# Kernel tuning notes

Measured on AMD Instinct MI355X. Metric: run time of the kernel, lower is better.

The kernel has to match this reference:

```python
import jax, jax.numpy as jnp
import numpy as np

F = 16        # num_frames
K = 8         # num_tokens (top-k)
SIZE = 64     # basis size
PD = 256      # prompt_dim
ED = 768      # embed_dim
EPS = 1e-12

def _l2norm(v, axis=-1):
    n = jnp.sqrt(jnp.sum(v * v, axis=axis, keepdims=True))
    return v / jnp.maximum(n, EPS)

def setup_inputs() -> dict:
    key = jax.random.key(0)
    k1, k2, k3, k4 = jax.random.split(key, 4)
    B, N = 32, 197
    x = jax.random.normal(k1, (B, F * N, ED), dtype=jnp.float32)
    # prompt_values ~ U(-1, 1), shape [size, 1, prompt_dim]
    prompt_values = jax.random.uniform(k2, (SIZE, 1, PD), dtype=jnp.float32, minval=-1.0, maxval=1.0)
    # prompt_inproj: Linear(embed_dim, prompt_dim, bias=False)
    W_in = jax.random.normal(k3, (PD, ED), dtype=jnp.float32) * (1.0 / np.sqrt(ED))
    # prompt_outproj: Linear(prompt_dim, embed_dim, bias=False), kaiming fan_out
    W_out = jax.random.normal(k4, (ED, PD), dtype=jnp.float32) * np.sqrt(2.0 / ED)
    return {"x": x, "W_in": W_in, "W_out": W_out, "prompt_values": prompt_values}

def reference(x, W_in, W_out, prompt_values):
    B = x.shape[0]
    x = jax.lax.stop_gradient(x)                       # x.detach()
    xf = x.reshape(B, F, -1, ED).mean(axis=2)          # [B, F, ED]
    query = jnp.einsum('bfe,pe->bfp', xf, W_in)        # prompt_inproj
    BZ = B * F
    q = _l2norm(query.reshape(BZ, PD), axis=1)         # [BZ, PD]
    keys = _l2norm(prompt_values.mean(axis=1), axis=1) # [SIZE, PD]
    sim = q @ keys.T                                   # [BZ, SIZE]
    # eval routing: top-k by similarity (argsort descending [:, :k])
    _, idx = jax.lax.top_k(sim, K)                     # [BZ, K] int32
    prompts = prompt_values[idx.reshape(-1)].reshape(BZ, K, PD)
    prompts = _l2norm(prompts, axis=-1)
    sel_sim = jnp.take_along_axis(sim, idx, axis=1)    # [BZ, K]
    sel_key = keys[idx]                                # [BZ, K, PD]
    recon = jnp.einsum('bk,bkd->bd', sel_sim, sel_key) # [BZ, PD]
    diff = jnp.sum((recon - jax.lax.stop_gradient(q)) ** 2) / BZ
    ksim = jnp.sum(jnp.abs(keys @ keys.T - jnp.eye(SIZE, dtype=keys.dtype))) / BZ
    ps = diff + ksim
    # rearrange '(b f) p d -> b (f p) d' then outproj
    out_prompts = prompts.reshape(B, F * K, PD)
    out_prompts = jnp.einsum('bnd,ed->bne', out_prompts, W_out)  # [B, F*K, ED]
    ps_loss = jnp.zeros((1,), dtype=x.dtype) + ps * F
    return out_prompts, ps_loss
```

## Files before the change

### kernel.cpp

```cpp
#include <hip/hip_runtime.h>

#define Ff 16
#define Kk 8
#define SIZEk 64
#define PDd 256
#define EDd 768
#define Nn 197
#define BZz 512
#define NPROD 64
#define RB  256
#define ED4 192
#define PD4 64
#define OUT_LOSS ((size_t)32 * 128 * EDd)
#define LOSS_SCALE (1.0f / 32.0f)
#define MAGIC 0x5A17EC0Du

__global__ __launch_bounds__(256, 2) void k_all(const float4* __restrict__ x,
                                                const float* __restrict__ Win,
                                                const float* __restrict__ Wout,
                                                const float* __restrict__ pv,
                                                float* __restrict__ keys,
                                                float* __restrict__ KW,
                                                unsigned* __restrict__ slots,
                                                float* __restrict__ out) {
    int blk = blockIdx.x, t = threadIdx.x;

    if (blk < NPROD) {
        __shared__ float ks[PDd];
        __shared__ float redp[4];
        __shared__ float s_norm;
        int s = blk;
        float v  = pv[(size_t)s * PDd + t];
        float sq = v * v;
        for (int o = 32; o > 0; o >>= 1) sq += __shfl_down(sq, o);
        if ((t & 63) == 0) redp[t >> 6] = sq;
        __syncthreads();
        if (t == 0) s_norm = fmaxf(sqrtf(redp[0] + redp[1] + redp[2] + redp[3]), 1e-12f);
        __syncthreads();
        float kv = v / s_norm;
        ks[t] = kv;
        keys[(size_t)s * PDd + t] = kv;
        __syncthreads();

        for (int r = 0; r < 3; r++) {
            int e = t + 256 * r;
            const float4* w  = (const float4*)(Wout + (size_t)e * PDd);
            const float4* k4 = (const float4*)ks;
            float d = 0.f;
            for (int i = 0; i < PD4; i++) {
                float4 wv = w[i]; float4 kvv = k4[i];
                d += wv.x * kvv.x + wv.y * kvv.y + wv.z * kvv.z + wv.w * kvv.w;
            }
            KW[(size_t)s * EDd + e] = d;
        }
        if (s == 0 && t == 0) out[OUT_LOSS] = 0.0f;
        __syncthreads();
        if (t == 0)
            __hip_atomic_store(&slots[s], MAGIC, __ATOMIC_RELEASE, __HIP_MEMORY_SCOPE_AGENT);

        if (t < SIZEk) {
            while (__hip_atomic_load(&slots[t], __ATOMIC_ACQUIRE, __HIP_MEMORY_SCOPE_AGENT)
                   != MAGIC)
                __builtin_amdgcn_s_sleep(8);
        }
        __syncthreads();
        if (t < SIZEk) {
            const float4* a = (const float4*)(keys + (size_t)s * PDd);
            const float4* b = (const float4*)(keys + (size_t)t * PDd);
            float d = 0.f;
            for (int c = 0; c < PD4; c++) {
                float4 av = a[c], bv = b[c];
                d += av.x * bv.x + av.y * bv.y + av.z * bv.z + av.w * bv.w;
            }
            float vv = fabsf(d - (s == t ? 1.0f : 0.0f));
            for (int o = 32; o > 0; o >>= 1) vv += __shfl_down(vv, o);
            if (t == 0) atomicAdd(out + OUT_LOSS, vv * LOSS_SCALE);
        }
        return;
    }

    __shared__ float xs[2][EDd];
    __shared__ float qs[2][PDd];
    __shared__ int   s_idx[2][Kk];
    __shared__ float s_sim[2][Kk];
    __shared__ float red[2][4];
    int bz0 = (blk - NPROD) * 2;

    if (t < ED4) {
        const float4* b0 = x + (size_t)bz0 * Nn * ED4;
        const float4* b1 = b0 + (size_t)Nn * ED4;
        float4 s0 = make_float4(0.f, 0.f, 0.f, 0.f);
        float4 s1 = make_float4(0.f, 0.f, 0.f, 0.f);
        int n = 0;
        for (; n + 4 <= Nn; n += 4) {
            float4 a0 = b0[(n + 0) * ED4 + t];
            float4 a1 = b0[(n + 1) * ED4 + t];
            float4 a2 = b0[(n + 2) * ED4 + t];
            float4 a3 = b0[(n + 3) * ED4 + t];
            float4 c0 = b1[(n + 0) * ED4 + t];
            float4 c1 = b1[(n + 1) * ED4 + t];
            float4 c2 = b1[(n + 2) * ED4 + t];
            float4 c3 = b1[(n + 3) * ED4 + t];
            s0.x += (a0.x + a1.x) + (a2.x + a3.x);
            s0.y += (a0.y + a1.y) + (a2.y + a3.y);
            s0.z += (a0.z + a1.z) + (a2.z + a3.z);
            s0.w += (a0.w + a1.w) + (a2.w + a3.w);
            s1.x += (c0.x + c1.x) + (c2.x + c3.x);
            s1.y += (c0.y + c1.y) + (c2.y + c3.y);
            s1.z += (c0.z + c1.z) + (c2.z + c3.z);
            s1.w += (c0.w + c1.w) + (c2.w + c3.w);
        }
        for (; n < Nn; n++) {
            float4 a = b0[n * ED4 + t];
            float4 c = b1[n * ED4 + t];
            s0.x += a.x; s0.y += a.y; s0.z += a.z; s0.w += a.w;
            s1.x += c.x; s1.y += c.y; s1.z += c.z; s1.w += c.w;
        }
        const float inv = 1.0f / (float)Nn;
        s0.x *= inv; s0.y *= inv; s0.z *= inv; s0.w *= inv;
        s1.x *= inv; s1.y *= inv; s1.z *= inv; s1.w *= inv;
        ((float4*)xs[0])[t] = s0;
        ((float4*)xs[1])[t] = s1;
    }
    __syncthreads();

    {
        const float4* w  = (const float4*)Win + (size_t)t * ED4;
        const float4* x0 = (const float4*)xs[0];
        const float4* x1 = (const float4*)xs[1];
        float d0 = 0.f, d1 = 0.f;
        for (int i = 0; i < ED4; i++) {
            float4 wv = w[i];
            float4 u0 = x0[i], u1 = x1[i];
            d0 += wv.x * u0.x + wv.y * u0.y + wv.z * u0.z + wv.w * u0.w;
            d1 += wv.x * u1.x + wv.y * u1.y + wv.z * u1.z + wv.w * u1.w;
        }
        float sq0 = d0 * d0, sq1 = d1 * d1;
        for (int o = 32; o > 0; o >>= 1) {
            sq0 += __shfl_down(sq0, o);
            sq1 += __shfl_down(sq1, o);
        }
        if ((t & 63) == 0) { red[0][t >> 6] = sq0; red[1][t >> 6] = sq1; }
        __syncthreads();
        float n0 = fmaxf(sqrtf(red[0][0] + red[0][1] + red[0][2] + red[0][3]), 1e-12f);
        float n1 = fmaxf(sqrtf(red[1][0] + red[1][1] + red[1][2] + red[1][3]), 1e-12f);
        qs[0][t] = d0 / n0;
        qs[1][t] = d1 / n1;
    }

    if (t < SIZEk) {
        while (__hip_atomic_load(&slots[t], __ATOMIC_ACQUIRE, __HIP_MEMORY_SCOPE_AGENT)
               != MAGIC)
            __builtin_amdgcn_s_sleep(8);
    }
    __syncthreads();

    if (t < 2 * SIZEk) {
        int row  = t >> 6;
        int lane = t & 63;
        const float4* kr = (const float4*)(keys + (size_t)lane * PDd);
        const float4* qr = (const float4*)qs[row];
        float d = 0.f;
        for (int c = 0; c < PD4; c++) {
            float4 a = kr[c], b = qr[c];
            d += a.x * b.x + a.y * b.y + a.z * b.z + a.w * b.w;
        }
        float v = d;
        for (int k = 0; k < Kk; k++) {
            float mv = v; int mi = lane;
            for (int o = 32; o > 0; o >>= 1) {
                float ov = __shfl_xor(mv, o);
                int   oi = __shfl_xor(mi, o);
                if (ov > mv || (ov == mv && oi < mi)) { mv = ov; mi = oi; }
            }
            if (lane == 0) { s_idx[row][k] = mi; s_sim[row][k] = mv; }
            if (lane == mi) v = -3e38f;
        }
    }
    __syncthreads();

    {
        float r0 = 0.f, r1 = 0.f;
        for (int k = 0; k < Kk; k++) {
            r0 += s_sim[0][k] * keys[(size_t)s_idx[0][k] * PDd + t];
            r1 += s_sim[1][k] * keys[(size_t)s_idx[1][k] * PDd + t];
        }
        float e0 = r0 - qs[0][t];
        float e1 = r1 - qs[1][t];
        float sq = e0 * e0 + e1 * e1;
        for (int o = 32; o > 0; o >>= 1) sq += __shfl_down(sq, o);
        if ((t & 63) == 0) red[0][t >> 6] = sq;
        __syncthreads();
        if (t == 0) atomicAdd(out + OUT_LOSS,
                              (red[0][0] + red[0][1] + red[0][2] + red[0][3]) * LOSS_SCALE);
    }

    float4* orow = (float4*)out + (size_t)bz0 * Kk * ED4;
    for (int i = t; i < 2 * Kk * ED4; i += 256) {
        int which = i / ED4;
        int e4    = i - which * ED4;
        int idx   = s_idx[which >> 3][which & 7];
        orow[i] = ((const float4*)(KW + (size_t)idx * EDd))[e4];
    }
}

extern "C" void kernel_launch(void* const* d_in, const int* in_sizes, int n_in,
                              void* d_out, int out_size, void* d_ws, size_t ws_size,
                              hipStream_t stream) {
    const float* x    = (const float*)d_in[0];
    const float* Win  = (const float*)d_in[1];
    const float* Wout = (const float*)d_in[2];
    const float* pv   = (const float*)d_in[3];
    float* out = (float*)d_out;
    float* ws  = (float*)d_ws;

    float*    keys  = ws;
    float*    KW    = ws + 16384;
    unsigned* slots = (unsigned*)(ws + 65536);

    k_all<<<NPROD + RB, 256, 0, stream>>>((const float4*)x, Win, Wout, pv,
                                          keys, KW, slots, out);
}
```

Baseline: 470.1 us.

## Assign one frame per block and use all 256 threads for mean reduction

```diff
diff --git a/kernel.cpp b/kernel.cpp
--- a/kernel.cpp
+++ b/kernel.cpp
@@ -1,19 +1,24 @@
 #include <hip/hip_runtime.h>
 
-#define Ff 16
 #define Kk 8
 #define SIZEk 64
 #define PDd 256
 #define EDd 768
 #define Nn 197
-#define BZz 512
 #define NPROD 64
-#define RB  256
+#define NR 512
 #define ED4 192
 #define PD4 64
+#define TOT4 (Nn * ED4)
+#define JFULL (TOT4 / 256)
+#define JMAIN (JFULL - (JFULL % 6))
 #define OUT_LOSS ((size_t)32 * 128 * EDd)
 #define LOSS_SCALE (1.0f / 32.0f)
 #define MAGIC 0x5A17EC0Du
+
+__device__ __forceinline__ void acc4(float4& s, float4 a) {
+    s.x += a.x; s.y += a.y; s.z += a.z; s.w += a.w;
+}
 
 __global__ __launch_bounds__(256, 2) void k_all(const float4* __restrict__ x,
                                                 const float* __restrict__ Win,
@@ -79,73 +84,67 @@
         return;
     }
 
-    __shared__ float xs[2][EDd];
-    __shared__ float qs[2][PDd];
-    __shared__ int   s_idx[2][Kk];
-    __shared__ float s_sim[2][Kk];
-    __shared__ float red[2][4];
-    int bz0 = (blk - NPROD) * 2;
-
+    __shared__ float4 part[4][ED4];
+    __shared__ float4 xs4[ED4];
+    __shared__ float4 qs4[PD4];
+    __shared__ int    s_idx[Kk];
+    __shared__ float  s_sim[Kk];
+    __shared__ float  red[4];
+    int bz = blk - NPROD;
+
+    {
+        const float4* base = x + (size_t)bz * TOT4;
+        float4 a0 = make_float4(0.f, 0.f, 0.f, 0.f);
+        float4 a1 = a0, a2 = a0;
+        int j = 0;
+        for (; j < JMAIN; j += 6) {
+            const float4* p = base + (size_t)j * 256 + t;
+            float4 v0 = p[0 * 256], v1 = p[1 * 256], v2 = p[2 * 256];
+            float4 v3 = p[3 * 256], v4 = p[4 * 256], v5 = p[5 * 256];
+            acc4(a0, v0); acc4(a1, v1); acc4(a2, v2);
+            acc4(a0, v3); acc4(a1, v4); acc4(a2, v5);
+        }
+        int f = JMAIN * 256 + t;
+        if (f < TOT4) acc4(a0, base[f]); f += 256;
+        if (f < TOT4) acc4(a1, base[f]); f += 256;
+        if (f < TOT4) acc4(a2, base[f]); f += 256;
+        if (f < TOT4) acc4(a0, base[f]);
+
+        int k  = t >> 6;
+        int c0 = t % ED4;
+        int c1 = (t + 64) % ED4;
+        int c2 = (t + 128) % ED4;
+        part[k][c0] = a0;
+        part[k][c1] = a1;
+        part[k][c2] = a2;
+    }
+    __syncthreads();
     if (t < ED4) {
-        const float4* b0 = x + (size_t)bz0 * Nn * ED4;
-        const float4* b1 = b0 + (size_t)Nn * ED4;
-        float4 s0 = make_float4(0.f, 0.f, 0.f, 0.f);
-        float4 s1 = make_float4(0.f, 0.f, 0.f, 0.f);
-        int n = 0;
-        for (; n + 4 <= Nn; n += 4) {
-            float4 a0 = b0[(n + 0) * ED4 + t];
-            float4 a1 = b0[(n + 1) * ED4 + t];
-            float4 a2 = b0[(n + 2) * ED4 + t];
-            float4 a3 = b0[(n + 3) * ED4 + t];
-            float4 c0 = b1[(n + 0) * ED4 + t];
-            float4 c1 = b1[(n + 1) * ED4 + t];
-            float4 c2 = b1[(n + 2) * ED4 + t];
-            float4 c3 = b1[(n + 3) * ED4 + t];
-            s0.x += (a0.x + a1.x) + (a2.x + a3.x);
-            s0.y += (a0.y + a1.y) + (a2.y + a3.y);
-            s0.z += (a0.z + a1.z) + (a2.z + a3.z);
-            s0.w += (a0.w + a1.w) + (a2.w + a3.w);
-            s1.x += (c0.x + c1.x) + (c2.x + c3.x);
-            s1.y += (c0.y + c1.y) + (c2.y + c3.y);
-            s1.z += (c0.z + c1.z) + (c2.z + c3.z);
-            s1.w += (c0.w + c1.w) + (c2.w + c3.w);
-        }
-        for (; n < Nn; n++) {
-            float4 a = b0[n * ED4 + t];
-            float4 c = b1[n * ED4 + t];
-            s0.x += a.x; s0.y += a.y; s0.z += a.z; s0.w += a.w;
-            s1.x += c.x; s1.y += c.y; s1.z += c.z; s1.w += c.w;
-        }
+        float4 s = part[0][t];
+        acc4(s, part[1][t]); acc4(s, part[2][t]); acc4(s, part[3][t]);
         const float inv = 1.0f / (float)Nn;
-        s0.x *= inv; s0.y *= inv; s0.z *= inv; s0.w *= inv;
-        s1.x *= inv; s1.y *= inv; s1.z *= inv; s1.w *= inv;
-        ((float4*)xs[0])[t] = s0;
-        ((float4*)xs[1])[t] = s1;
-    }
-    __syncthreads();
-
+        xs4[t] = make_float4(s.x * inv, s.y * inv, s.z * inv, s.w * inv);
+    }
+    __syncthreads();
+
+    float qv;
     {
-        const float4* w  = (const float4*)Win + (size_t)t * ED4;
-        const float4* x0 = (const float4*)xs[0];
-        const float4* x1 = (const float4*)xs[1];
-        float d0 = 0.f, d1 = 0.f;
-        for (int i = 0; i < ED4; i++) {
-            float4 wv = w[i];
-            float4 u0 = x0[i], u1 = x1[i];
-            d0 += wv.x * u0.x + wv.y * u0.y + wv.z * u0.z + wv.w * u0.w;
-            d1 += wv.x * u1.x + wv.y * u1.y + wv.z * u1.z + wv.w * u1.w;
-        }
-        float sq0 = d0 * d0, sq1 = d1 * d1;
-        for (int o = 32; o > 0; o >>= 1) {
-            sq0 += __shfl_down(sq0, o);
-            sq1 += __shfl_down(sq1, o);
-        }
-        if ((t & 63) == 0) { red[0][t >> 6] = sq0; red[1][t >> 6] = sq1; }
-        __syncthreads();
-        float n0 = fmaxf(sqrtf(red[0][0] + red[0][1] + red[0][2] + red[0][3]), 1e-12f);
-        float n1 = fmaxf(sqrtf(red[1][0] + red[1][1] + red[1][2] + red[1][3]), 1e-12f);
-        qs[0][t] = d0 / n0;
-        qs[1][t] = d1 / n1;
+        const float4* w = (const float4*)Win + (size_t)t * ED4;
+        float da = 0.f, db = 0.f;
+        for (int i = 0; i < ED4; i += 2) {
+            float4 w0 = w[i], w1 = w[i + 1];
+            float4 u0 = xs4[i], u1 = xs4[i + 1];
+            da += w0.x * u0.x + w0.y * u0.y + w0.z * u0.z + w0.w * u0.w;
+            db += w1.x * u1.x + w1.y * u1.y + w1.z * u1.z + w1.w * u1.w;
+        }
+        float d0 = da + db;
+        float sq = d0 * d0;
+        for (int o = 32; o > 0; o >>= 1) sq += __shfl_down(sq, o);
+        if ((t & 63) == 0) red[t >> 6] = sq;
+        __syncthreads();
+        float n0 = fmaxf(sqrtf(red[0] + red[1] + red[2] + red[3]), 1e-12f);
+        qv = d0 / n0;
+        ((float*)qs4)[t] = qv;
     }
 
     if (t < SIZEk) {
@@ -155,14 +154,12 @@
     }
     __syncthreads();
 
-    if (t < 2 * SIZEk) {
-        int row  = t >> 6;
-        int lane = t & 63;
+    if (t < SIZEk) {
+        int lane = t;
         const float4* kr = (const float4*)(keys + (size_t)lane * PDd);
-        const float4* qr = (const float4*)qs[row];
         float d = 0.f;
         for (int c = 0; c < PD4; c++) {
-            float4 a = kr[c], b = qr[c];
+            float4 a = kr[c], b = qs4[c];
             d += a.x * b.x + a.y * b.y + a.z * b.z + a.w * b.w;
         }
         float v = d;
@@ -173,33 +170,30 @@
                 int   oi = __shfl_xor(mi, o);
                 if (ov > mv || (ov == mv && oi < mi)) { mv = ov; mi = oi; }
             }
-            if (lane == 0) { s_idx[row][k] = mi; s_sim[row][k] = mv; }
+            if (lane == 0) { s_idx[k] = mi; s_sim[k] = mv; }
             if (lane == mi) v = -3e38f;
         }
     }
     __syncthreads();
 
     {
-        float r0 = 0.f, r1 = 0.f;
-        for (int k = 0; k < Kk; k++) {
-            r0 += s_sim[0][k] * keys[(size_t)s_idx[0][k] * PDd + t];
-            r1 += s_sim[1][k] * keys[(size_t)s_idx[1][k] * PDd + t];
-        }
-        float e0 = r0 - qs[0][t];
-        float e1 = r1 - qs[1][t];
-        float sq = e0 * e0 + e1 * e1;
+        float r = 0.f;
+        for (int k = 0; k < Kk; k++)
+            r += s_sim[k] * keys[(size_t)s_idx[k] * PDd + t];
+        float e = r - qv;
+        float sq = e * e;
         for (int o = 32; o > 0; o >>= 1) sq += __shfl_down(sq, o);
-        if ((t & 63) == 0) red[0][t >> 6] = sq;
+        if ((t & 63) == 0) red[t >> 6] = sq;
         __syncthreads();
         if (t == 0) atomicAdd(out + OUT_LOSS,
-                              (red[0][0] + red[0][1] + red[0][2] + red[0][3]) * LOSS_SCALE);
-    }
-
-    float4* orow = (float4*)out + (size_t)bz0 * Kk * ED4;
-    for (int i = t; i < 2 * Kk * ED4; i += 256) {
+                              (red[0] + red[1] + red[2] + red[3]) * LOSS_SCALE);
+    }
+
+    float4* orow = (float4*)out + (size_t)bz * Kk * ED4;
+    for (int i = t; i < Kk * ED4; i += 256) {
         int which = i / ED4;
         int e4    = i - which * ED4;
-        int idx   = s_idx[which >> 3][which & 7];
+        int idx   = s_idx[which];
         orow[i] = ((const float4*)(KW + (size_t)idx * EDd))[e4];
     }
 }
@@ -218,6 +212,6 @@
     float*    KW    = ws + 16384;
     unsigned* slots = (unsigned*)(ws + 65536);
 
-    k_all<<<NPROD + RB, 256, 0, stream>>>((const float4*)x, Win, Wout, pv,
+    k_all<<<NPROD + NR, 256, 0, stream>>>((const float4*)x, Win, Wout, pv,
                                           keys, KW, slots, out);
 }
```

Result: slower. 524.0 us (+11.5%).
